# Optimization experiments

Hardware: AMD Instinct MI355X
Metric: run time of the kernel (lower is better)

## Reference

```python
import jax, jax.numpy as jnp
import numpy as np

LN_EPS = 1e-5


def setup_inputs() -> dict:
    key = jax.random.key(0)
    ks = jax.random.split(key, 10)
    N, E, D, H = 32000, 512000, 256, 128
    atom_features = jax.random.normal(ks[0], (N, D), dtype=jnp.float32)
    edge_features = jax.random.normal(ks[1], (E, H), dtype=jnp.float32)
    edge_index = jax.random.randint(ks[2], (2, E), 0, N, dtype=jnp.int64)
    s = lambda fan_in: 1.0 / np.sqrt(fan_in)
    W_lin = jax.random.normal(ks[3], (D, H), dtype=jnp.float32) * s(D)
    W1 = jax.random.normal(ks[4], (3 * H, H), dtype=jnp.float32) * s(3 * H)
    b1 = jnp.zeros((H,), jnp.float32)
    W2 = jax.random.normal(ks[5], (H, H), dtype=jnp.float32) * s(H)
    b2 = jnp.zeros((H,), jnp.float32)
    W3 = jax.random.normal(ks[6], (H, H), dtype=jnp.float32) * s(H)
    b3 = jnp.zeros((H,), jnp.float32)
    gamma = jnp.ones((H,), jnp.float32)
    beta = jnp.zeros((H,), jnp.float32)
    return dict(atom_features=atom_features, edge_features=edge_features,
                edge_index=edge_index, W_lin=W_lin, W1=W1, b1=b1, W2=W2,
                b2=b2, W3=W3, b3=b3, gamma=gamma, beta=beta)


def _layernorm(x, gamma, beta):
    mu = jnp.mean(x, axis=-1, keepdims=True)
    var = jnp.mean((x - mu) ** 2, axis=-1, keepdims=True)
    return (x - mu) * jax.lax.rsqrt(var + LN_EPS) * gamma + beta


def reference(atom_features, edge_features, edge_index, W_lin, W1, b1, W2, b2, W3, b3, gamma, beta):
    # o3.Linear on scalar irreps -> plain bias-free linear: [N, D] @ [D, H]
    atom_scalars = atom_features @ W_lin  # [N, H]
    edge_dst, edge_src = edge_index[0], edge_index[1]
    # gather + concat: [E, 3H]
    edge_in = jnp.concatenate(
        [atom_scalars[edge_dst], atom_scalars[edge_src], edge_features], axis=-1)
    h = jax.nn.relu(edge_in @ W1 + b1)
    h = jax.nn.relu(h @ W2 + b2)
    h = h @ W3 + b3  # [E, H]
    return _layernorm(edge_features + h, gamma, beta)
```

## Files before the change

kernel.cpp:

```cpp
#include <hip/hip_runtime.h>

typedef __attribute__((ext_vector_type(8))) short bf16x8;
typedef __attribute__((ext_vector_type(16))) float f32x16;
typedef __attribute__((ext_vector_type(4))) float f32x4;
typedef __attribute__((ext_vector_type(4))) unsigned u32x4;

#define LN_EPS 1e-5f

__device__ __forceinline__ unsigned short f2bf(float f) {
    unsigned u = __float_as_uint(f);
    unsigned r = (u + 0x7FFFu + ((u >> 16) & 1u)) >> 16;
    return (unsigned short)r;
}

__device__ __forceinline__ unsigned cvt_pk_bf16(float lo, float hi) {
    unsigned r;
    asm("v_cvt_pk_bf16_f32 %0, %1, %2" : "=v"(r) : "v"(lo), "v"(hi));
    return r;
}

__device__ __forceinline__ void permswap(unsigned& a, unsigned& b) {
    asm("v_permlane32_swap_b32 %0, %1" : "+v"(a), "+v"(b));
}

__global__ void prep_weights(const float* __restrict__ W_lin,
                             const float* __restrict__ W1,
                             const float* __restrict__ W2,
                             const float* __restrict__ W3,
                             unsigned short* __restrict__ wt_lin,
                             unsigned short* __restrict__ wimg) {
    int i = blockIdx.x * blockDim.x + threadIdx.x;
    if (i < 128 * 256) {
        int n = i >> 8, k = i & 255;
        wt_lin[n * 256 + k] = f2bf(W_lin[k * 128 + n]);
    } else if (i < 128 * 256 + 5 * 16384) {
        int j = i - 128 * 256;
        int mat = j >> 14, r = j & 16383;
        int jj = r & 7, l = (r >> 3) & 63, ks = (r >> 9) & 7, f = r >> 12;
        int n = 32 * f + (l & 31);
        int k = 16 * ks + 8 * (l >> 5) + jj;
        float v;
        if (mat < 3)       v = W1[(mat * 128 + k) * 128 + n];
        else if (mat == 3) v = W2[k * 128 + n];
        else               v = W3[k * 128 + n];
        wimg[j] = f2bf(v);
    }
}

__global__ void atoms_gemm(const float* __restrict__ af,
                           const unsigned short* __restrict__ wt_lin,
                           unsigned short* __restrict__ atoms_bf,
                           int Natoms) {
    const int wv = threadIdx.x >> 6, lane = threadIdx.x & 63;
    const int l31 = lane & 31, g8 = (lane >> 5) * 8, g4 = (lane >> 5) * 4;
    const int R = blockIdx.x * 128 + wv * 32;

    f32x16 acc[4];
#pragma unroll
    for (int f = 0; f < 4; ++f)
#pragma unroll
        for (int e = 0; e < 16; ++e) acc[f][e] = 0.0f;

    int arow = R + l31;
    if (arow >= Natoms) arow = Natoms - 1;
    const float* ap = af + (size_t)arow * 256;

#pragma unroll
    for (int ks = 0; ks < 16; ++ks) {
        const int k0 = ks * 16 + g8;
        float4 x0 = *(const float4*)(ap + k0);
        float4 x1 = *(const float4*)(ap + k0 + 4);
        bf16x8 a;
        a[0] = (short)f2bf(x0.x); a[1] = (short)f2bf(x0.y);
        a[2] = (short)f2bf(x0.z); a[3] = (short)f2bf(x0.w);
        a[4] = (short)f2bf(x1.x); a[5] = (short)f2bf(x1.y);
        a[6] = (short)f2bf(x1.z); a[7] = (short)f2bf(x1.w);
#pragma unroll
        for (int f = 0; f < 4; ++f) {
            bf16x8 b = *(const bf16x8*)(wt_lin + (32 * f + l31) * 256 + k0);
            acc[f] = __builtin_amdgcn_mfma_f32_32x32x16_bf16(a, b, acc[f], 0, 0, 0);
        }
    }

#pragma unroll
    for (int f = 0; f < 4; ++f) {
        const int col = 32 * f + l31;
#pragma unroll
        for (int r = 0; r < 16; ++r) {
            int row = R + (r & 3) + 8 * (r >> 2) + g4;
            if (row < Natoms) atoms_bf[(size_t)row * 128 + col] = f2bf(acc[f][r]);
        }
    }
}

__global__ __launch_bounds__(1024, 4) void edge_fused(
    const float* __restrict__ ef, const int* __restrict__ eidx,
    const unsigned short* __restrict__ atoms_bf,
    const unsigned short* __restrict__ wimg,
    const float* __restrict__ b1, const float* __restrict__ b2,
    const float* __restrict__ b3, const float* __restrict__ gamma_,
    const float* __restrict__ beta_, float* __restrict__ out, int E) {
    __shared__ unsigned short wlds[4 * 16384];

    const int tid = threadIdx.x;
    const int lane = tid & 63, wv = tid >> 6;
    const int l31 = lane & 31, hi = lane >> 5, h8 = hi * 8;

    {
        const char* s = (const char*)wimg;
        char* d = (char*)wlds;
        const int o = tid * 16;
#pragma unroll
        for (int i = 0; i < 8; ++i)
            __builtin_amdgcn_global_load_lds(
                (const __attribute__((address_space(1))) unsigned int*)(s + o + i * 16384),
                (__attribute__((address_space(3))) unsigned int*)(d + o + i * 16384),
                16, 0, 0);
    }

    const int e0 = blockIdx.x * 512 + wv * 32 + l31;
    const int e = e0 < E ? e0 : E - 1;
    const int dI = eidx[e], sI = eidx[E + e];
    const unsigned short* dRow = atoms_bf + (size_t)dI * 128;
    const unsigned short* sRow = atoms_bf + (size_t)sI * 128;
    const float* efRow = ef + (size_t)e * 128;

    bf16x8 gd[8];
#pragma unroll
    for (int ks = 0; ks < 8; ++ks)
        gd[ks] = *(const bf16x8*)(dRow + ks * 16 + h8);

    f32x16 acc[4];
    auto initb = [&](const float* __restrict__ bb) {
#pragma unroll
        for (int f = 0; f < 4; ++f)
#pragma unroll
            for (int m = 0; m < 4; ++m) {
                f32x4 b4 = *(const f32x4*)(bb + 32 * f + 8 * m + 4 * hi);
#pragma unroll
                for (int i = 0; i < 4; ++i) acc[f][4 * m + i] = b4[i];
            }
    };

    bf16x8 frag[8];
    auto build_frags = [&]() {
#pragma unroll
        for (int f = 0; f < 4; ++f) {
            unsigned pk0[4], pk1[4];
#pragma unroll
            for (int m = 0; m < 4; ++m) {
                float a0 = fmaxf(acc[f][4 * m + 0], 0.0f);
                float a1 = fmaxf(acc[f][4 * m + 1], 0.0f);
                float a2 = fmaxf(acc[f][4 * m + 2], 0.0f);
                float a3 = fmaxf(acc[f][4 * m + 3], 0.0f);
                pk0[m] = cvt_pk_bf16(a0, a1);
                pk1[m] = cvt_pk_bf16(a2, a3);
            }
#pragma unroll
            for (int k1 = 0; k1 < 2; ++k1) {
                unsigned x0 = pk0[2 * k1], y0 = pk0[2 * k1 + 1];
                unsigned x1 = pk1[2 * k1], y1 = pk1[2 * k1 + 1];
                permswap(x0, y0);
                permswap(x1, y1);
                union { u32x4 u; bf16x8 b; } cv;
                cv.u = (u32x4){x0, x1, y0, y1};
                frag[2 * f + k1] = cv.b;
            }
        }
    };

    const unsigned short* lbase = wlds + lane * 8;
    const unsigned short* wg3 = wimg + 4 * 16384 + lane * 8;

    __syncthreads();

    initb(b1);
#pragma unroll
    for (int ks = 0; ks < 8; ++ks) {
#pragma unroll
        for (int f = 0; f < 4; ++f) {
            bf16x8 a = *(const bf16x8*)(lbase + ((0 * 4 + f) * 8 + ks) * 512);
            acc[f] = __builtin_amdgcn_mfma_f32_32x32x16_bf16(a, gd[ks], acc[f], 0, 0, 0);
        }
    }
#pragma unroll
    for (int ks = 0; ks < 8; ++ks) {
        bf16x8 bx = *(const bf16x8*)(sRow + ks * 16 + h8);
#pragma unroll
        for (int f = 0; f < 4; ++f) {
            bf16x8 a = *(const bf16x8*)(lbase + ((1 * 4 + f) * 8 + ks) * 512);
            acc[f] = __builtin_amdgcn_mfma_f32_32x32x16_bf16(a, bx, acc[f], 0, 0, 0);
        }
    }
#pragma unroll
    for (int ks = 0; ks < 8; ++ks) {
        f32x4 x0 = *(const f32x4*)(efRow + ks * 16 + h8);
        f32x4 x1 = *(const f32x4*)(efRow + ks * 16 + h8 + 4);
        union { u32x4 u; bf16x8 b; } cv;
        cv.u = (u32x4){cvt_pk_bf16(x0[0], x0[1]), cvt_pk_bf16(x0[2], x0[3]),
                       cvt_pk_bf16(x1[0], x1[1]), cvt_pk_bf16(x1[2], x1[3])};
#pragma unroll
        for (int f = 0; f < 4; ++f) {
            bf16x8 a = *(const bf16x8*)(lbase + ((2 * 4 + f) * 8 + ks) * 512);
            acc[f] = __builtin_amdgcn_mfma_f32_32x32x16_bf16(a, cv.b, acc[f], 0, 0, 0);
        }
    }

    build_frags();
    initb(b2);
#pragma unroll
    for (int ks = 0; ks < 8; ++ks)
#pragma unroll
        for (int f = 0; f < 4; ++f) {
            bf16x8 a = *(const bf16x8*)(lbase + ((3 * 4 + f) * 8 + ks) * 512);
            acc[f] = __builtin_amdgcn_mfma_f32_32x32x16_bf16(a, frag[ks], acc[f], 0, 0, 0);
        }

    build_frags();
    initb(b3);
#pragma unroll
    for (int ks = 0; ks < 8; ++ks)
#pragma unroll
        for (int f = 0; f < 4; ++f) {
            bf16x8 a = *(const bf16x8*)(wg3 + (f * 8 + ks) * 512);
            acc[f] = __builtin_amdgcn_mfma_f32_32x32x16_bf16(a, frag[ks], acc[f], 0, 0, 0);
        }

    float s = 0.0f, q = 0.0f;
#pragma unroll
    for (int f = 0; f < 4; ++f)
#pragma unroll
        for (int m = 0; m < 4; ++m) {
            f32x4 r4 = *(const f32x4*)(efRow + 32 * f + 8 * m + 4 * hi);
#pragma unroll
            for (int i = 0; i < 4; ++i) {
                float v = acc[f][4 * m + i] + r4[i];
                acc[f][4 * m + i] = v;
                s += v;
                q += v * v;
            }
        }
    s += __shfl_xor(s, 32, 64);
    q += __shfl_xor(q, 32, 64);
    const float mu = s * (1.0f / 128.0f);
    const float var = q * (1.0f / 128.0f) - mu * mu;
    const float rs = rsqrtf(var + LN_EPS);

    if (e0 < E) {
        float* orow = out + (size_t)e0 * 128;
#pragma unroll
        for (int f = 0; f < 4; ++f)
#pragma unroll
            for (int m = 0; m < 4; ++m) {
                f32x4 g4 = *(const f32x4*)(gamma_ + 32 * f + 8 * m + 4 * hi);
                f32x4 be4 = *(const f32x4*)(beta_ + 32 * f + 8 * m + 4 * hi);
                f32x4 o;
#pragma unroll
                for (int i = 0; i < 4; ++i)
                    o[i] = (acc[f][4 * m + i] - mu) * rs * g4[i] + be4[i];
                *(f32x4*)(orow + 32 * f + 8 * m + 4 * hi) = o;
            }
    }
}

extern "C" void kernel_launch(void* const* d_in, const int* in_sizes, int n_in,
                              void* d_out, int out_size, void* d_ws, size_t ws_size,
                              hipStream_t stream) {
    const float* atom_features = (const float*)d_in[0];
    const float* edge_features = (const float*)d_in[1];
    const int* edge_index = (const int*)d_in[2];
    const float* W_lin = (const float*)d_in[3];
    const float* W1 = (const float*)d_in[4];
    const float* b1 = (const float*)d_in[5];
    const float* W2 = (const float*)d_in[6];
    const float* b2 = (const float*)d_in[7];
    const float* W3 = (const float*)d_in[8];
    const float* b3 = (const float*)d_in[9];
    const float* gamma_ = (const float*)d_in[10];
    const float* beta_ = (const float*)d_in[11];
    float* out = (float*)d_out;

    const int Natoms = in_sizes[0] / 256;
    const int E = in_sizes[1] / 128;

    unsigned short* atoms_bf = (unsigned short*)d_ws;
    unsigned short* wt_lin = atoms_bf + (size_t)Natoms * 128;
    unsigned short* wimg = wt_lin + 128 * 256;

    const int prep_items = 128 * 256 + 5 * 16384;
    prep_weights<<<(prep_items + 255) / 256, 256, 0, stream>>>(W_lin, W1, W2, W3,
                                                               wt_lin, wimg);
    atoms_gemm<<<(Natoms + 127) / 128, 256, 0, stream>>>(atom_features, wt_lin,
                                                         atoms_bf, Natoms);
    edge_fused<<<(E + 511) / 512, 1024, 0, stream>>>(edge_features, edge_index,
                                                     atoms_bf, wimg, b1, b2, b3,
                                                     gamma_, beta_, out, E);
}
```

Measured before the change: 269.8 us.

## Prefetch all edge gathers upfront, keep residual in bf16 registers, halve block size

```diff
diff --git a/kernel.cpp b/kernel.cpp
--- a/kernel.cpp
+++ b/kernel.cpp
@@ -93,7 +93,7 @@
     }
 }
 
-__global__ __launch_bounds__(1024, 4) void edge_fused(
+__global__ __launch_bounds__(512, 2) void edge_fused(
     const float* __restrict__ ef, const int* __restrict__ eidx,
     const unsigned short* __restrict__ atoms_bf,
     const unsigned short* __restrict__ wimg,
@@ -111,24 +111,45 @@
         char* d = (char*)wlds;
         const int o = tid * 16;
 #pragma unroll
-        for (int i = 0; i < 8; ++i)
+        for (int i = 0; i < 16; ++i)
             __builtin_amdgcn_global_load_lds(
-                (const __attribute__((address_space(1))) unsigned int*)(s + o + i * 16384),
-                (__attribute__((address_space(3))) unsigned int*)(d + o + i * 16384),
+                (const __attribute__((address_space(1))) unsigned int*)(s + o + i * 8192),
+                (__attribute__((address_space(3))) unsigned int*)(d + o + i * 8192),
                 16, 0, 0);
     }
 
-    const int e0 = blockIdx.x * 512 + wv * 32 + l31;
+    const int e0 = blockIdx.x * 256 + wv * 32 + l31;
     const int e = e0 < E ? e0 : E - 1;
     const int dI = eidx[e], sI = eidx[E + e];
     const unsigned short* dRow = atoms_bf + (size_t)dI * 128;
     const unsigned short* sRow = atoms_bf + (size_t)sI * 128;
     const float* efRow = ef + (size_t)e * 128;
 
-    bf16x8 gd[8];
-#pragma unroll
-    for (int ks = 0; ks < 8; ++ks)
+    bf16x8 gd[8], gs[8];
+#pragma unroll
+    for (int ks = 0; ks < 8; ++ks) {
         gd[ks] = *(const bf16x8*)(dRow + ks * 16 + h8);
+        gs[ks] = *(const bf16x8*)(sRow + ks * 16 + h8);
+    }
+    bf16x8 efc[8];
+#pragma unroll
+    for (int ks = 0; ks < 8; ++ks) {
+        f32x4 x0 = *(const f32x4*)(efRow + ks * 16 + h8);
+        f32x4 x1 = *(const f32x4*)(efRow + ks * 16 + h8 + 4);
+        union { u32x4 u; bf16x8 b; } cv;
+        cv.u = (u32x4){cvt_pk_bf16(x0[0], x0[1]), cvt_pk_bf16(x0[2], x0[3]),
+                       cvt_pk_bf16(x1[0], x1[1]), cvt_pk_bf16(x1[2], x1[3])};
+        efc[ks] = cv.b;
+    }
+    unsigned efr[32];
+#pragma unroll
+    for (int f = 0; f < 4; ++f)
+#pragma unroll
+        for (int m = 0; m < 4; ++m) {
+            f32x4 r = *(const f32x4*)(efRow + 32 * f + 8 * m + 4 * hi);
+            efr[2 * (4 * f + m) + 0] = cvt_pk_bf16(r[0], r[1]);
+            efr[2 * (4 * f + m) + 1] = cvt_pk_bf16(r[2], r[3]);
+        }
 
     f32x16 acc[4];
     auto initb = [&](const float* __restrict__ bb) {
@@ -185,24 +206,18 @@
     }
 #pragma unroll
     for (int ks = 0; ks < 8; ++ks) {
-        bf16x8 bx = *(const bf16x8*)(sRow + ks * 16 + h8);
 #pragma unroll
         for (int f = 0; f < 4; ++f) {
             bf16x8 a = *(const bf16x8*)(lbase + ((1 * 4 + f) * 8 + ks) * 512);
-            acc[f] = __builtin_amdgcn_mfma_f32_32x32x16_bf16(a, bx, acc[f], 0, 0, 0);
-        }
-    }
-#pragma unroll
-    for (int ks = 0; ks < 8; ++ks) {
-        f32x4 x0 = *(const f32x4*)(efRow + ks * 16 + h8);
-        f32x4 x1 = *(const f32x4*)(efRow + ks * 16 + h8 + 4);
-        union { u32x4 u; bf16x8 b; } cv;
-        cv.u = (u32x4){cvt_pk_bf16(x0[0], x0[1]), cvt_pk_bf16(x0[2], x0[3]),
-                       cvt_pk_bf16(x1[0], x1[1]), cvt_pk_bf16(x1[2], x1[3])};
+            acc[f] = __builtin_amdgcn_mfma_f32_32x32x16_bf16(a, gs[ks], acc[f], 0, 0, 0);
+        }
+    }
+#pragma unroll
+    for (int ks = 0; ks < 8; ++ks) {
 #pragma unroll
         for (int f = 0; f < 4; ++f) {
             bf16x8 a = *(const bf16x8*)(lbase + ((2 * 4 + f) * 8 + ks) * 512);
-            acc[f] = __builtin_amdgcn_mfma_f32_32x32x16_bf16(a, cv.b, acc[f], 0, 0, 0);
+            acc[f] = __builtin_amdgcn_mfma_f32_32x32x16_bf16(a, efc[ks], acc[f], 0, 0, 0);
         }
     }
 
@@ -231,14 +246,20 @@
     for (int f = 0; f < 4; ++f)
 #pragma unroll
         for (int m = 0; m < 4; ++m) {
-            f32x4 r4 = *(const f32x4*)(efRow + 32 * f + 8 * m + 4 * hi);
-#pragma unroll
-            for (int i = 0; i < 4; ++i) {
-                float v = acc[f][4 * m + i] + r4[i];
-                acc[f][4 * m + i] = v;
-                s += v;
-                q += v * v;
-            }
+            const unsigned w0 = efr[2 * (4 * f + m) + 0];
+            const unsigned w1 = efr[2 * (4 * f + m) + 1];
+            float r0 = __uint_as_float(w0 << 16);
+            float r1 = __uint_as_float(w0 & 0xffff0000u);
+            float r2 = __uint_as_float(w1 << 16);
+            float r3 = __uint_as_float(w1 & 0xffff0000u);
+            float v0 = acc[f][4 * m + 0] + r0;
+            float v1 = acc[f][4 * m + 1] + r1;
+            float v2 = acc[f][4 * m + 2] + r2;
+            float v3 = acc[f][4 * m + 3] + r3;
+            acc[f][4 * m + 0] = v0; acc[f][4 * m + 1] = v1;
+            acc[f][4 * m + 2] = v2; acc[f][4 * m + 3] = v3;
+            s += v0 + v1 + v2 + v3;
+            q += v0 * v0 + v1 * v1 + v2 * v2 + v3 * v3;
         }
     s += __shfl_xor(s, 32, 64);
     q += __shfl_xor(q, 32, 64);
@@ -292,7 +313,7 @@
                                                                wt_lin, wimg);
     atoms_gemm<<<(Natoms + 127) / 128, 256, 0, stream>>>(atom_features, wt_lin,
                                                          atoms_bf, Natoms);
-    edge_fused<<<(E + 511) / 512, 1024, 0, stream>>>(edge_features, edge_index,
-                                                     atoms_bf, wimg, b1, b2, b3,
-                                                     gamma_, beta_, out, E);
-}
+    edge_fused<<<(E + 255) / 256, 512, 0, stream>>>(edge_features, edge_index,
+                                                    atoms_bf, wimg, b1, b2, b3,
+                                                    gamma_, beta_, out, E);
+}
```

Measured after the change: 326.8 us. 21.2% more time.
